# Optimization experiments

Measured on AMD Instinct MI355X. Metric: run time of the kernel, lower is better.

Reference implementation:

```python
import jax, jax.numpy as jnp
import numpy as np

SQRT_N = 128  # n = SQRT_N**2 = 16384


def setup_inputs() -> dict:
    key = jax.random.key(0)
    k1, k2, k3 = jax.random.split(key, 3)
    x = jax.random.normal(k1, (4, 1024, SQRT_N * SQRT_N), dtype=jnp.float32)
    L = jax.random.normal(k2, (SQRT_N, SQRT_N, SQRT_N), dtype=jnp.float32)
    R = jax.random.normal(k3, (SQRT_N, SQRT_N, SQRT_N), dtype=jnp.float32)
    return {"x": x, "L": L, "R": R}


def reference(x, L, R):
    s = L.shape[0]
    orig_shape = x.shape
    # view last dim as (m, n) with m = n = sqrt_n
    X = x.reshape(*orig_shape[:-1], s, s)
    # rearrange '... (m n) -> ... (n m)': transpose the two factors
    X = X.swapaxes(-1, -2)           # [..., b=s, m=s] blocks along axis -2
    # block-diagonal matmul with L: einsum 'bnm,...bm->...bn'
    X = jnp.einsum('bnm,...bm->...bn', L, X)
    # rearrange again (flatten (b,n) then split (m,n) is identity, so transpose)
    X = X.swapaxes(-1, -2)
    # block-diagonal matmul with R
    X = jnp.einsum('bnm,...bm->...bn', R, X)
    # final rearrange '... (m n) -> ... (n m)'
    X = X.swapaxes(-1, -2)
    return X.reshape(orig_shape)
```

## Files before the change

kernel.cpp:

```cpp
#include <hip/hip_runtime.h>
#include <hip/hip_bf16.h>

#define SDIM 128
#define NCOL 16384
#define ROWS_TOTAL 4096
#define CHUNK 1024
#define RT_PC 64
#define NCHUNK 4

using bf16x8 = __attribute__((ext_vector_type(8))) __bf16;
using su8    = __attribute__((ext_vector_type(8))) ushort;
using f32x4  = __attribute__((ext_vector_type(4))) float;

__device__ __forceinline__ ushort f2bf(float f) {
  __hip_bfloat16 h = __float2bfloat16(f);
  union { __hip_bfloat16 h; ushort u; } c; c.h = h;
  return c.u;
}

__global__ __launch_bounds__(256) void k_prep(const float* __restrict__ L,
                                              const float* __restrict__ R,
                                              ushort* __restrict__ Lt,
                                              ushort* __restrict__ Rt) {
  int id = blockIdx.x * 256 + threadIdx.x;
  const float* in = (id < 262144) ? L : R;
  ushort* outp    = (id < 262144) ? Lt : Rt;
  int t  = id & 262143;
  int t1 = t >> 11;
  int ks = (t >> 9) & 3;
  int tb = (t >> 6) & 7;
  int g  = (t >> 4) & 3;
  int tl = t & 15;
  const float* src = in + (size_t)(t1 * 128 + tb * 16 + tl) * 128 + ks * 32 + g * 8;
  float4 a = *reinterpret_cast<const float4*>(src);
  float4 b = *reinterpret_cast<const float4*>(src + 4);
  su8 o;
  o[0] = f2bf(a.x); o[1] = f2bf(a.y); o[2] = f2bf(a.z); o[3] = f2bf(a.w);
  o[4] = f2bf(b.x); o[5] = f2bf(b.y); o[6] = f2bf(b.z); o[7] = f2bf(b.w);
  *reinterpret_cast<su8*>(outp + (size_t)t * 8) = o;
}

__global__ __launch_bounds__(512, 2) void k_s1(const float* __restrict__ x,
                                               const ushort* __restrict__ Lt,
                                               ushort* __restrict__ T3) {
  __shared__ __align__(16) ushort sh[32768];
  int tid = threadIdx.x;
  unsigned bid = blockIdx.x;
  int mg2 = bid & 7;
  int rt  = bid >> 3;
  int row0 = rt * 16;
  int m0 = mg2 * 16;

  {
    int r  = tid >> 5;
    int q  = tid & 3;
    int k8 = (tid >> 2) & 7;
    const float* base = x + (size_t)(row0 + r) * NCOL + (size_t)(k8 * 16) * SDIM + m0 + q * 4;
    ushort vm[4][16];
#pragma unroll
    for (int kk = 0; kk < 16; ++kk) {
      float4 a = *reinterpret_cast<const float4*>(base + (size_t)kk * SDIM);
      vm[0][kk] = f2bf(a.x); vm[1][kk] = f2bf(a.y);
      vm[2][kk] = f2bf(a.z); vm[3][kk] = f2bf(a.w);
    }
    int swz_w = (r & 7) << 3;
#pragma unroll
    for (int mm = 0; mm < 4; ++mm) {
      int mloc = q * 4 + mm;
      int ebase = ((mloc * 16 + r) << 7) + k8 * 16;
      su8 lo, hi;
#pragma unroll
      for (int e = 0; e < 8; ++e) { lo[e] = vm[mm][e]; hi[e] = vm[mm][8 + e]; }
      *reinterpret_cast<su8*>(&sh[ebase ^ swz_w]) = lo;
      *reinterpret_cast<su8*>(&sh[(ebase + 8) ^ swz_w]) = hi;
    }
  }
  __syncthreads();

  int wave = tid >> 6, lane = tid & 63;
  int l15 = lane & 15, g = lane >> 4;
  int swz = (l15 & 7) << 3;
  int w4 = wave & 3, mgh = wave >> 2;
  int m0h = m0 + mgh * 8;
  const ushort* Lp = Lt + ((size_t)m0h * 32 + (size_t)w4 * 2) * 512 + (size_t)lane * 8;

  f32x4 st[2][8];
#pragma unroll
  for (int m = 0; m < 8; ++m) {
    int mloc = mgh * 8 + m;
    bf16x8 xf[4];
#pragma unroll
    for (int ks = 0; ks < 4; ++ks) {
      int e = ((mloc * 16 + l15) << 7) + ks * 32 + g * 8;
      xf[ks] = *reinterpret_cast<const bf16x8*>(&sh[e ^ swz]);
    }
    f32x4 a0 = {0.f, 0.f, 0.f, 0.f};
    f32x4 a1 = {0.f, 0.f, 0.f, 0.f};
#pragma unroll
    for (int ks = 0; ks < 4; ++ks) {
      bf16x8 l0 = *reinterpret_cast<const bf16x8*>(Lp + (size_t)((m * 4 + ks) * 8 + 0) * 512);
      bf16x8 l1 = *reinterpret_cast<const bf16x8*>(Lp + (size_t)((m * 4 + ks) * 8 + 1) * 512);
      a0 = __builtin_amdgcn_mfma_f32_16x16x32_bf16(xf[ks], l0, a0, 0, 0, 0);
      a1 = __builtin_amdgcn_mfma_f32_16x16x32_bf16(xf[ks], l1, a1, 0, 0, 0);
    }
    st[0][m] = a0;
    st[1][m] = a1;
  }

  __syncthreads();
#pragma unroll
  for (int jt = 0; jt < 2; ++jt) {
    int j = w4 * 32 + jt * 16 + l15;
#pragma unroll
    for (int v = 0; v < 4; ++v) {
      int slot = (g * 4 + v) ^ ((j & 3) << 1);
      su8 o;
      o[0] = f2bf(st[jt][0][v]); o[1] = f2bf(st[jt][1][v]);
      o[2] = f2bf(st[jt][2][v]); o[3] = f2bf(st[jt][3][v]);
      o[4] = f2bf(st[jt][4][v]); o[5] = f2bf(st[jt][5][v]);
      o[6] = f2bf(st[jt][6][v]); o[7] = f2bf(st[jt][7][v]);
      *reinterpret_cast<su8*>(&sh[(((size_t)j * 2 + mgh) * 16 + slot) * 8]) = o;
    }
  }
  __syncthreads();
#pragma unroll
  for (int it = 0; it < 8; ++it) {
    int task = it * 512 + tid;
    int j    = task >> 5;
    int unit = task & 31;
    int mghc = unit >> 4;
    int slot = unit & 15;
    int mgc  = mg2 * 2 + mghc;
    int ks1c = mgc >> 2, g2c = mgc & 3;
    const ushort* sl = &sh[(((size_t)j * 2 + mghc) * 16 + (slot ^ ((j & 3) << 1))) * 8];
    size_t a = (((size_t)(rt * 128 + j) * 4 + ks1c) * 64 + g2c * 16 + slot) * 8;
    *reinterpret_cast<su8*>(T3 + a) = *reinterpret_cast<const su8*>(sl);
  }
}

__global__ __launch_bounds__(512, 4) void k_s2(const ushort* __restrict__ T3,
                                               const ushort* __restrict__ Rt,
                                               float* __restrict__ out) {
  __shared__ __align__(16) ushort sh[16384];
  int tid = threadIdx.x;
  unsigned bid = blockIdx.x;
  int jg = bid & 7;
  int rt = bid >> 3;
  int row0 = rt * 16;
  int j0 = jg * 16;

  int wave = tid >> 6, lane = tid & 63;
  int l15 = lane & 15, g = lane >> 4;
  int ibase = wave * 16;

  const ushort* s = T3 + (size_t)(rt * 128 + j0) * 4 * 512;
  const ushort* Rp = Rt + ((size_t)j0 * 32 + wave) * 512 + (size_t)lane * 8;
  const ushort* tp = sh + (size_t)lane * 8;

  f32x4 acc[16];
#pragma unroll
  for (int jj = 0; jj < 16; ++jj) acc[jj] = {0.f, 0.f, 0.f, 0.f};

#pragma unroll
  for (int h = 0; h < 2; ++h) {
    if (h) __syncthreads();
#if __has_builtin(__builtin_amdgcn_global_load_lds)
#pragma unroll
    for (int q = 0; q < 4; ++q) {
      int src_off = (h * 4 + q) * 512 + tid;
      int dst_off = q * 512 + tid;
      __builtin_amdgcn_global_load_lds(
          (const __attribute__((address_space(1))) unsigned int*)(s + (size_t)src_off * 8),
          (__attribute__((address_space(3))) unsigned int*)(sh + (size_t)dst_off * 8),
          16, 0, 0);
    }
#else
    {
      const su8* s8 = reinterpret_cast<const su8*>(s);
      su8* d8 = reinterpret_cast<su8*>(sh);
#pragma unroll
      for (int q = 0; q < 4; ++q)
        d8[q * 512 + tid] = s8[(h * 4 + q) * 512 + tid];
    }
#endif
    __syncthreads();
#pragma unroll
    for (int jl = 0; jl < 8; ++jl) {
      int jj = h * 8 + jl;
#pragma unroll
      for (int ks = 0; ks < 4; ++ks) {
        bf16x8 af = *reinterpret_cast<const bf16x8*>(tp + (size_t)(jl * 4 + ks) * 512);
        bf16x8 bf = *reinterpret_cast<const bf16x8*>(Rp + (size_t)(jj * 32 + ks * 8) * 512);
        acc[jj] = __builtin_amdgcn_mfma_f32_16x16x32_bf16(af, bf, acc[jj], 0, 0, 0);
      }
    }
  }

  float* shf = reinterpret_cast<float*>(sh);
#pragma unroll
  for (int ph = 0; ph < 4; ++ph) {
    __syncthreads();
    {
      int i = ibase + l15;
      float* dl = shf + ((size_t)g * 128 + i) * 16;
#pragma unroll
      for (int q = 0; q < 4; ++q) {
        f32x4 o; o[0] = acc[q * 4 + 0][ph]; o[1] = acc[q * 4 + 1][ph];
                 o[2] = acc[q * 4 + 2][ph]; o[3] = acc[q * 4 + 3][ph];
        *reinterpret_cast<f32x4*>(dl + ((q ^ (i & 3)) * 4)) = o;
      }
    }
    __syncthreads();
#pragma unroll
    for (int it = 0; it < 4; ++it) {
      int task = it * 512 + tid;
      int rs = task >> 9;
      int rem = task & 511;
      int i = rem >> 2;
      int q = rem & 3;
      int row = row0 + rs * 4 + ph;
      const float* sl = shf + ((size_t)rs * 128 + i) * 16 + ((q ^ (i & 3)) * 4);
      float* dg = out + (size_t)row * NCOL + (size_t)i * SDIM + j0 + q * 4;
      *reinterpret_cast<f32x4*>(dg) = *reinterpret_cast<const f32x4*>(sl);
    }
  }
}

extern "C" void kernel_launch(void* const* d_in, const int* in_sizes, int n_in,
                              void* d_out, int out_size, void* d_ws, size_t ws_size,
                              hipStream_t stream) {
  const float* x = (const float*)d_in[0];
  const float* L = (const float*)d_in[1];
  const float* R = (const float*)d_in[2];
  float* out = (float*)d_out;

  ushort* Lt = (ushort*)d_ws;
  ushort* Rt = Lt + 2097152;
  ushort* T3 = Rt + 2097152;

  k_prep<<<2048, 256, 0, stream>>>(L, R, Lt, Rt);

  for (int c = 0; c < NCHUNK; ++c) {
    const float* xc = x + (size_t)c * CHUNK * NCOL;
    float* oc = out + (size_t)c * CHUNK * NCOL;
    k_s1<<<dim3(RT_PC * 8), 512, 0, stream>>>(xc, Lt, T3);
    k_s2<<<dim3(RT_PC * 8), 512, 0, stream>>>(T3, Rt, oc);
  }
}
```

Measured before the change: 249.5 us.

## Halve k_s1 shared memory by splitting K into two phases for higher occupancy

Stage 1 now loads and converts the x tile in two K halves, reusing a 32 KB LDS buffer in place of a single 64 KB load. Accumulators persist across both halves. The epilogue writes back one m-half at a time so it fits the smaller buffer. This lets launch bounds request 4 blocks per CU to hide memory latency, at the cost of extra barriers and serialized epilogue phases.

```diff
diff --git a/kernel.cpp b/kernel.cpp
--- a/kernel.cpp
+++ b/kernel.cpp
@@ -40,10 +40,10 @@
   *reinterpret_cast<su8*>(outp + (size_t)t * 8) = o;
 }
 
-__global__ __launch_bounds__(512, 2) void k_s1(const float* __restrict__ x,
+__global__ __launch_bounds__(512, 4) void k_s1(const float* __restrict__ x,
                                                const ushort* __restrict__ Lt,
                                                ushort* __restrict__ T3) {
-  __shared__ __align__(16) ushort sh[32768];
+  __shared__ __align__(16) ushort sh[16384];
   int tid = threadIdx.x;
   unsigned bid = blockIdx.x;
   int mg2 = bid & 7;
@@ -51,32 +51,6 @@
   int row0 = rt * 16;
   int m0 = mg2 * 16;
 
-  {
-    int r  = tid >> 5;
-    int q  = tid & 3;
-    int k8 = (tid >> 2) & 7;
-    const float* base = x + (size_t)(row0 + r) * NCOL + (size_t)(k8 * 16) * SDIM + m0 + q * 4;
-    ushort vm[4][16];
-#pragma unroll
-    for (int kk = 0; kk < 16; ++kk) {
-      float4 a = *reinterpret_cast<const float4*>(base + (size_t)kk * SDIM);
-      vm[0][kk] = f2bf(a.x); vm[1][kk] = f2bf(a.y);
-      vm[2][kk] = f2bf(a.z); vm[3][kk] = f2bf(a.w);
-    }
-    int swz_w = (r & 7) << 3;
-#pragma unroll
-    for (int mm = 0; mm < 4; ++mm) {
-      int mloc = q * 4 + mm;
-      int ebase = ((mloc * 16 + r) << 7) + k8 * 16;
-      su8 lo, hi;
-#pragma unroll
-      for (int e = 0; e < 8; ++e) { lo[e] = vm[mm][e]; hi[e] = vm[mm][8 + e]; }
-      *reinterpret_cast<su8*>(&sh[ebase ^ swz_w]) = lo;
-      *reinterpret_cast<su8*>(&sh[(ebase + 8) ^ swz_w]) = hi;
-    }
-  }
-  __syncthreads();
-
   int wave = tid >> 6, lane = tid & 63;
   int l15 = lane & 15, g = lane >> 4;
   int swz = (l15 & 7) << 3;
@@ -86,55 +60,91 @@
 
   f32x4 st[2][8];
 #pragma unroll
-  for (int m = 0; m < 8; ++m) {
-    int mloc = mgh * 8 + m;
-    bf16x8 xf[4];
-#pragma unroll
-    for (int ks = 0; ks < 4; ++ks) {
-      int e = ((mloc * 16 + l15) << 7) + ks * 32 + g * 8;
-      xf[ks] = *reinterpret_cast<const bf16x8*>(&sh[e ^ swz]);
-    }
-    f32x4 a0 = {0.f, 0.f, 0.f, 0.f};
-    f32x4 a1 = {0.f, 0.f, 0.f, 0.f};
-#pragma unroll
-    for (int ks = 0; ks < 4; ++ks) {
-      bf16x8 l0 = *reinterpret_cast<const bf16x8*>(Lp + (size_t)((m * 4 + ks) * 8 + 0) * 512);
-      bf16x8 l1 = *reinterpret_cast<const bf16x8*>(Lp + (size_t)((m * 4 + ks) * 8 + 1) * 512);
-      a0 = __builtin_amdgcn_mfma_f32_16x16x32_bf16(xf[ks], l0, a0, 0, 0, 0);
-      a1 = __builtin_amdgcn_mfma_f32_16x16x32_bf16(xf[ks], l1, a1, 0, 0, 0);
-    }
-    st[0][m] = a0;
-    st[1][m] = a1;
-  }
-
-  __syncthreads();
-#pragma unroll
-  for (int jt = 0; jt < 2; ++jt) {
-    int j = w4 * 32 + jt * 16 + l15;
-#pragma unroll
-    for (int v = 0; v < 4; ++v) {
-      int slot = (g * 4 + v) ^ ((j & 3) << 1);
-      su8 o;
-      o[0] = f2bf(st[jt][0][v]); o[1] = f2bf(st[jt][1][v]);
-      o[2] = f2bf(st[jt][2][v]); o[3] = f2bf(st[jt][3][v]);
-      o[4] = f2bf(st[jt][4][v]); o[5] = f2bf(st[jt][5][v]);
-      o[6] = f2bf(st[jt][6][v]); o[7] = f2bf(st[jt][7][v]);
-      *reinterpret_cast<su8*>(&sh[(((size_t)j * 2 + mgh) * 16 + slot) * 8]) = o;
-    }
-  }
-  __syncthreads();
-#pragma unroll
-  for (int it = 0; it < 8; ++it) {
-    int task = it * 512 + tid;
-    int j    = task >> 5;
-    int unit = task & 31;
-    int mghc = unit >> 4;
-    int slot = unit & 15;
-    int mgc  = mg2 * 2 + mghc;
+  for (int jt = 0; jt < 2; ++jt)
+#pragma unroll
+    for (int m = 0; m < 8; ++m) st[jt][m] = {0.f, 0.f, 0.f, 0.f};
+
+#pragma unroll
+  for (int kh = 0; kh < 2; ++kh) {
+    if (kh) __syncthreads();
+    {
+      int r   = tid >> 5;
+      int rem = tid & 31;
+      int k8  = rem >> 3;
+      int h2  = (rem >> 2) & 1;
+      int q   = rem & 3;
+      const float* base = x + (size_t)(row0 + r) * NCOL
+                            + (size_t)(kh * 64 + k8 * 16 + h2 * 8) * SDIM + m0 + q * 4;
+      ushort vm[4][8];
+#pragma unroll
+      for (int kk = 0; kk < 8; ++kk) {
+        float4 a = *reinterpret_cast<const float4*>(base + (size_t)kk * SDIM);
+        vm[0][kk] = f2bf(a.x); vm[1][kk] = f2bf(a.y);
+        vm[2][kk] = f2bf(a.z); vm[3][kk] = f2bf(a.w);
+      }
+      int swz_w = (r & 7) << 3;
+#pragma unroll
+      for (int mm = 0; mm < 4; ++mm) {
+        int mloc = q * 4 + mm;
+        int ebase = ((mloc * 16 + r) << 6) + k8 * 16 + h2 * 8;
+        su8 w;
+#pragma unroll
+        for (int e = 0; e < 8; ++e) w[e] = vm[mm][e];
+        *reinterpret_cast<su8*>(&sh[ebase ^ swz_w]) = w;
+      }
+    }
+    __syncthreads();
+#pragma unroll
+    for (int m = 0; m < 8; ++m) {
+      int mloc = mgh * 8 + m;
+      bf16x8 xf[2];
+#pragma unroll
+      for (int ksl = 0; ksl < 2; ++ksl) {
+        int e = ((mloc * 16 + l15) << 6) + ksl * 32 + g * 8;
+        xf[ksl] = *reinterpret_cast<const bf16x8*>(&sh[e ^ swz]);
+      }
+#pragma unroll
+      for (int ksl = 0; ksl < 2; ++ksl) {
+        int ks = kh * 2 + ksl;
+        bf16x8 l0 = *reinterpret_cast<const bf16x8*>(Lp + (size_t)((m * 4 + ks) * 8 + 0) * 512);
+        bf16x8 l1 = *reinterpret_cast<const bf16x8*>(Lp + (size_t)((m * 4 + ks) * 8 + 1) * 512);
+        st[0][m] = __builtin_amdgcn_mfma_f32_16x16x32_bf16(xf[ksl], l0, st[0][m], 0, 0, 0);
+        st[1][m] = __builtin_amdgcn_mfma_f32_16x16x32_bf16(xf[ksl], l1, st[1][m], 0, 0, 0);
+      }
+    }
+  }
+
+#pragma unroll
+  for (int eph = 0; eph < 2; ++eph) {
+    __syncthreads();
+    if (mgh == eph) {
+#pragma unroll
+      for (int jt = 0; jt < 2; ++jt) {
+        int j = w4 * 32 + jt * 16 + l15;
+#pragma unroll
+        for (int v = 0; v < 4; ++v) {
+          int slot = (g * 4 + v) ^ ((j & 3) << 1);
+          su8 o;
+          o[0] = f2bf(st[jt][0][v]); o[1] = f2bf(st[jt][1][v]);
+          o[2] = f2bf(st[jt][2][v]); o[3] = f2bf(st[jt][3][v]);
+          o[4] = f2bf(st[jt][4][v]); o[5] = f2bf(st[jt][5][v]);
+          o[6] = f2bf(st[jt][6][v]); o[7] = f2bf(st[jt][7][v]);
+          *reinterpret_cast<su8*>(&sh[((size_t)j * 16 + slot) * 8]) = o;
+        }
+      }
+    }
+    __syncthreads();
+    int mgc  = mg2 * 2 + eph;
     int ks1c = mgc >> 2, g2c = mgc & 3;
-    const ushort* sl = &sh[(((size_t)j * 2 + mghc) * 16 + (slot ^ ((j & 3) << 1))) * 8];
-    size_t a = (((size_t)(rt * 128 + j) * 4 + ks1c) * 64 + g2c * 16 + slot) * 8;
-    *reinterpret_cast<su8*>(T3 + a) = *reinterpret_cast<const su8*>(sl);
+#pragma unroll
+    for (int it = 0; it < 4; ++it) {
+      int task = it * 512 + tid;
+      int j    = task >> 4;
+      int slot = task & 15;
+      const ushort* sl = &sh[((size_t)j * 16 + (slot ^ ((j & 3) << 1))) * 8];
+      size_t a = (((size_t)(rt * 128 + j) * 4 + ks1c) * 64 + g2c * 16 + slot) * 8;
+      *reinterpret_cast<su8*>(T3 + a) = *reinterpret_cast<const su8*>(sl);
+    }
   }
 }
 
```

New measurement: 264.5 us. 1.06x slower.

## Process two row tiles per stage-1 block with register prefetch of next tile

Applied to the files above, without the earlier changes.

Each k_s1 block now handles two consecutive 16-row tiles. It loads the second tile's x values into registers while the first tile's MFMA compute and write-back run, so global load latency is overlapped with compute. The row chunk size is doubled so there are half as many kernel launches. This raises register pressure, halves the stage-1 grid per row, and doubles the intermediate T3 buffer footprint.

```diff
diff --git a/kernel.cpp b/kernel.cpp
--- a/kernel.cpp
+++ b/kernel.cpp
@@ -4,9 +4,8 @@
 #define SDIM 128
 #define NCOL 16384
 #define ROWS_TOTAL 4096
-#define CHUNK 1024
-#define RT_PC 64
-#define NCHUNK 4
+#define CHUNK 2048
+#define NCHUNK 2
 
 using bf16x8 = __attribute__((ext_vector_type(8))) __bf16;
 using su8    = __attribute__((ext_vector_type(8))) ushort;
@@ -40,51 +39,31 @@
   *reinterpret_cast<su8*>(outp + (size_t)t * 8) = o;
 }
 
-__global__ __launch_bounds__(512, 2) void k_s1(const float* __restrict__ x,
-                                               const ushort* __restrict__ Lt,
-                                               ushort* __restrict__ T3) {
-  __shared__ __align__(16) ushort sh[32768];
-  int tid = threadIdx.x;
-  unsigned bid = blockIdx.x;
-  int mg2 = bid & 7;
-  int rt  = bid >> 3;
-  int row0 = rt * 16;
-  int m0 = mg2 * 16;
-
-  {
-    int r  = tid >> 5;
-    int q  = tid & 3;
-    int k8 = (tid >> 2) & 7;
-    const float* base = x + (size_t)(row0 + r) * NCOL + (size_t)(k8 * 16) * SDIM + m0 + q * 4;
-    ushort vm[4][16];
-#pragma unroll
-    for (int kk = 0; kk < 16; ++kk) {
-      float4 a = *reinterpret_cast<const float4*>(base + (size_t)kk * SDIM);
-      vm[0][kk] = f2bf(a.x); vm[1][kk] = f2bf(a.y);
-      vm[2][kk] = f2bf(a.z); vm[3][kk] = f2bf(a.w);
-    }
-    int swz_w = (r & 7) << 3;
-#pragma unroll
-    for (int mm = 0; mm < 4; ++mm) {
-      int mloc = q * 4 + mm;
-      int ebase = ((mloc * 16 + r) << 7) + k8 * 16;
-      su8 lo, hi;
-#pragma unroll
-      for (int e = 0; e < 8; ++e) { lo[e] = vm[mm][e]; hi[e] = vm[mm][8 + e]; }
-      *reinterpret_cast<su8*>(&sh[ebase ^ swz_w]) = lo;
-      *reinterpret_cast<su8*>(&sh[(ebase + 8) ^ swz_w]) = hi;
-    }
-  }
-  __syncthreads();
-
-  int wave = tid >> 6, lane = tid & 63;
-  int l15 = lane & 15, g = lane >> 4;
-  int swz = (l15 & 7) << 3;
-  int w4 = wave & 3, mgh = wave >> 2;
-  int m0h = m0 + mgh * 8;
-  const ushort* Lp = Lt + ((size_t)m0h * 32 + (size_t)w4 * 2) * 512 + (size_t)lane * 8;
-
-  f32x4 st[2][8];
+__device__ __forceinline__ void s1_to_lds(ushort* sh, const float4* buf,
+                                          int r, int q, int k8) {
+  ushort vm[4][16];
+#pragma unroll
+  for (int kk = 0; kk < 16; ++kk) {
+    float4 a = buf[kk];
+    vm[0][kk] = f2bf(a.x); vm[1][kk] = f2bf(a.y);
+    vm[2][kk] = f2bf(a.z); vm[3][kk] = f2bf(a.w);
+  }
+  int swz_w = (r & 7) << 3;
+#pragma unroll
+  for (int mm = 0; mm < 4; ++mm) {
+    int mloc = q * 4 + mm;
+    int ebase = ((mloc * 16 + r) << 7) + k8 * 16;
+    su8 lo, hi;
+#pragma unroll
+    for (int e = 0; e < 8; ++e) { lo[e] = vm[mm][e]; hi[e] = vm[mm][8 + e]; }
+    *reinterpret_cast<su8*>(&sh[ebase ^ swz_w]) = lo;
+    *reinterpret_cast<su8*>(&sh[(ebase + 8) ^ swz_w]) = hi;
+  }
+}
+
+__device__ __forceinline__ void s1_compute(const ushort* sh, const ushort* Lp,
+                                           int l15, int g, int swz, int mgh,
+                                           f32x4 st[2][8]) {
 #pragma unroll
   for (int m = 0; m < 8; ++m) {
     int mloc = mgh * 8 + m;
@@ -106,7 +85,11 @@
     st[0][m] = a0;
     st[1][m] = a1;
   }
-
+}
+
+__device__ __forceinline__ void s1_bounce(ushort* sh, const f32x4 st[2][8],
+                                          int tid, int w4, int mgh, int l15, int g,
+                                          int mg2, int rt, ushort* __restrict__ T3) {
   __syncthreads();
 #pragma unroll
   for (int jt = 0; jt < 2; ++jt) {
@@ -138,6 +121,61 @@
   }
 }
 
+__global__ __launch_bounds__(512, 2) void k_s1(const float* __restrict__ x,
+                                               const ushort* __restrict__ Lt,
+                                               ushort* __restrict__ T3) {
+  __shared__ __align__(16) ushort sh[32768];
+  int tid = threadIdx.x;
+  unsigned bid = blockIdx.x;
+  int mg2 = bid & 7;
+  int rp  = bid >> 3;
+  int m0 = mg2 * 16;
+
+  int r  = tid >> 5;
+  int q  = tid & 3;
+  int k8 = (tid >> 2) & 7;
+  const float* base0 = x + (size_t)(rp * 32 + r) * NCOL + (size_t)(k8 * 16) * SDIM + m0 + q * 4;
+
+  int wave = tid >> 6, lane = tid & 63;
+  int l15 = lane & 15, g = lane >> 4;
+  int swz = (l15 & 7) << 3;
+  int w4 = wave & 3, mgh = wave >> 2;
+  int m0h = m0 + mgh * 8;
+  const ushort* Lp = Lt + ((size_t)m0h * 32 + (size_t)w4 * 2) * 512 + (size_t)lane * 8;
+
+  {
+    float4 b0[16];
+#pragma unroll
+    for (int kk = 0; kk < 16; ++kk)
+      b0[kk] = *reinterpret_cast<const float4*>(base0 + (size_t)kk * SDIM);
+    s1_to_lds(sh, b0, r, q, k8);
+  }
+  __syncthreads();
+
+  float4 b1[16];
+  {
+    const float* base1 = base0 + (size_t)16 * NCOL;
+#pragma unroll
+    for (int kk = 0; kk < 16; ++kk)
+      b1[kk] = *reinterpret_cast<const float4*>(base1 + (size_t)kk * SDIM);
+  }
+
+  {
+    f32x4 st[2][8];
+    s1_compute(sh, Lp, l15, g, swz, mgh, st);
+    s1_bounce(sh, st, tid, w4, mgh, l15, g, mg2, rp * 2, T3);
+  }
+
+  __syncthreads();
+  s1_to_lds(sh, b1, r, q, k8);
+  __syncthreads();
+  {
+    f32x4 st[2][8];
+    s1_compute(sh, Lp, l15, g, swz, mgh, st);
+    s1_bounce(sh, st, tid, w4, mgh, l15, g, mg2, rp * 2 + 1, T3);
+  }
+}
+
 __global__ __launch_bounds__(512, 4) void k_s2(const ushort* __restrict__ T3,
                                                const ushort* __restrict__ Rt,
                                                float* __restrict__ out) {
@@ -166,9 +204,9 @@
     if (h) __syncthreads();
 #if __has_builtin(__builtin_amdgcn_global_load_lds)
 #pragma unroll
-    for (int q = 0; q < 4; ++q) {
-      int src_off = (h * 4 + q) * 512 + tid;
-      int dst_off = q * 512 + tid;
+    for (int qq = 0; qq < 4; ++qq) {
+      int src_off = (h * 4 + qq) * 512 + tid;
+      int dst_off = qq * 512 + tid;
       __builtin_amdgcn_global_load_lds(
           (const __attribute__((address_space(1))) unsigned int*)(s + (size_t)src_off * 8),
           (__attribute__((address_space(3))) unsigned int*)(sh + (size_t)dst_off * 8),
@@ -179,8 +217,8 @@
       const su8* s8 = reinterpret_cast<const su8*>(s);
       su8* d8 = reinterpret_cast<su8*>(sh);
 #pragma unroll
-      for (int q = 0; q < 4; ++q)
-        d8[q * 512 + tid] = s8[(h * 4 + q) * 512 + tid];
+      for (int qq = 0; qq < 4; ++qq)
+        d8[qq * 512 + tid] = s8[(h * 4 + qq) * 512 + tid];
     }
 #endif
     __syncthreads();
@@ -204,10 +242,10 @@
       int i = ibase + l15;
       float* dl = shf + ((size_t)g * 128 + i) * 16;
 #pragma unroll
-      for (int q = 0; q < 4; ++q) {
-        f32x4 o; o[0] = acc[q * 4 + 0][ph]; o[1] = acc[q * 4 + 1][ph];
-                 o[2] = acc[q * 4 + 2][ph]; o[3] = acc[q * 4 + 3][ph];
-        *reinterpret_cast<f32x4*>(dl + ((q ^ (i & 3)) * 4)) = o;
+      for (int qq = 0; qq < 4; ++qq) {
+        f32x4 o; o[0] = acc[qq * 4 + 0][ph]; o[1] = acc[qq * 4 + 1][ph];
+                 o[2] = acc[qq * 4 + 2][ph]; o[3] = acc[qq * 4 + 3][ph];
+        *reinterpret_cast<f32x4*>(dl + ((qq ^ (i & 3)) * 4)) = o;
       }
     }
     __syncthreads();
@@ -217,10 +255,10 @@
       int rs = task >> 9;
       int rem = task & 511;
       int i = rem >> 2;
-      int q = rem & 3;
+      int qq = rem & 3;
       int row = row0 + rs * 4 + ph;
-      const float* sl = shf + ((size_t)rs * 128 + i) * 16 + ((q ^ (i & 3)) * 4);
-      float* dg = out + (size_t)row * NCOL + (size_t)i * SDIM + j0 + q * 4;
+      const float* sl = shf + ((size_t)rs * 128 + i) * 16 + ((qq ^ (i & 3)) * 4);
+      float* dg = out + (size_t)row * NCOL + (size_t)i * SDIM + j0 + qq * 4;
       *reinterpret_cast<f32x4*>(dg) = *reinterpret_cast<const f32x4*>(sl);
     }
   }
@@ -243,7 +281,7 @@
   for (int c = 0; c < NCHUNK; ++c) {
     const float* xc = x + (size_t)c * CHUNK * NCOL;
     float* oc = out + (size_t)c * CHUNK * NCOL;
-    k_s1<<<dim3(RT_PC * 8), 512, 0, stream>>>(xc, Lt, T3);
-    k_s2<<<dim3(RT_PC * 8), 512, 0, stream>>>(T3, Rt, oc);
-  }
-}
+    k_s1<<<dim3((CHUNK / 32) * 8), 512, 0, stream>>>(xc, Lt, T3);
+    k_s2<<<dim3((CHUNK / 16) * 8), 512, 0, stream>>>(T3, Rt, oc);
+  }
+}
```

Measured after the change: 288.3 us. 1.16x slower.
